# Kernel optimization log

Measured on AMD Instinct MI355X. Metric: run time of the kernel, lower is better.

The kernel has to match this reference:

```python
import jax, jax.numpy as jnp
import numpy as np

# ---- static config (mirrors module init / config constants) ----
STATE_DIM = 512
D_H = 2048
INPUT_DIM = 1024
N_QUBITS = 6
N_VQC_LAYERS = 3
MSD = 128                 # mamba_state_dim (last dim of padded state)
PAD_SLICES = 16           # padded slice count in h_padded
MIN_T = 1e-6              # control_limits.min_value
REL_STEP = 0.1            # control_limits.hardware_relative_step
ABS_STEP = 1e-4           # control_limits.hardware_absolute_step
MAX_T = 0.05              # control_limits.max_value
DIM = 2 ** N_QUBITS

# qubit 0 = most significant bit (matches reshape-based gate application)
_BITS = ((np.arange(DIM)[:, None] >> np.arange(N_QUBITS)[None, ::-1]) & 1).astype(np.float32)
_sign = np.ones(DIM, np.float32)
for k in range(N_QUBITS):  # ring CZ entanglement
    k2 = (k + 1) % N_QUBITS
    _sign *= 1.0 - 2.0 * _BITS[:, k] * _BITS[:, k2]
CZ_SIGN = jnp.asarray(_sign)
Z_OBS = jnp.asarray((1.0 - 2.0 * _BITS).mean(axis=1))  # mean <Z_k> observable weights


def _apply_ry(state, ang, k):
    # state: [B, 2^n] real statevector; ang: [B] rotation angle on qubit k
    B = state.shape[0]
    s = state.reshape(B, 2 ** k, 2, 2 ** (N_QUBITS - k - 1))
    c = jnp.cos(ang / 2)[:, None, None]
    si = jnp.sin(ang / 2)[:, None, None]
    a0, a1 = s[:, :, 0, :], s[:, :, 1, :]
    out = jnp.stack([c * a0 - si * a1, si * a0 + c * a1], axis=2)
    return out.reshape(B, DIM)


def _vqc(feats, enc_W, enc_b, thetas):
    # EvolutionTimeVQCLayer: angle-encode features, layered RY + ring CZ, mean-Z expectation
    B = feats.shape[0]
    angles = feats @ enc_W + enc_b  # [B, n_qubits]
    state = jnp.zeros((B, DIM), feats.dtype).at[:, 0].set(1.0)
    for k in range(N_QUBITS):
        state = _apply_ry(state, angles[:, k], k)
    for l in range(N_VQC_LAYERS):
        for k in range(N_QUBITS):
            state = _apply_ry(state, jnp.broadcast_to(thetas[l, k], (B,)), k)
        state = state * CZ_SIGN[None, :]
    return (state * state) @ Z_OBS  # [B]


def _hamiltonian(q, p, x, W1, b1, W2, b2, W3, b3):
    z = jnp.concatenate([q, p, x], axis=-1)          # [B, 2*S + D]
    h1 = jnp.tanh(z @ W1 + b1)
    h2 = jnp.tanh(h1 @ W2 + b2)
    return (h2 @ W3)[:, 0] + b3                       # [B] scalar energy per sample


def setup_inputs() -> dict:
    key = jax.random.key(0)
    ks = jax.random.split(key, 12)
    def glorot(k, shape):
        std = np.sqrt(2.0 / (shape[0] + shape[-1]))
        return jax.random.normal(k, shape, jnp.float32) * std
    B = 2048
    h_in = 2 * STATE_DIM + INPUT_DIM
    gen_in = INPUT_DIM + 2 * STATE_DIM
    return {
        'x': jax.random.normal(ks[0], (B, INPUT_DIM), jnp.float32),
        'h_padded': jax.random.normal(ks[1], (B, PAD_SLICES, MSD), jnp.float32),
        'aux_padded': jnp.zeros((B, PAD_SLICES, MSD), jnp.float32),
        'W1': glorot(ks[2], (h_in, D_H)), 'b1': jnp.zeros((D_H,), jnp.float32),
        'W2': glorot(ks[3], (D_H, D_H)), 'b2': jnp.zeros((D_H,), jnp.float32),
        'W3': glorot(ks[4], (D_H, 1)), 'b3': jnp.zeros((), jnp.float32),
        'W_out': glorot(ks[5], (2 * STATE_DIM, INPUT_DIM)),
        'b_out': jnp.zeros((INPUT_DIM,), jnp.float32),
        'enc_W': glorot(ks[6], (gen_in, N_QUBITS)) * 0.1,
        'enc_b': jnp.zeros((N_QUBITS,), jnp.float32),
        'thetas': jax.random.normal(ks[7], (N_VQC_LAYERS, N_QUBITS), jnp.float32) * 0.1,
        'gain': jnp.asarray(0.1, jnp.float32),
        'shift': jnp.asarray(7.0, jnp.float32),
        'cap_param': jnp.asarray(0.02, jnp.float32),
        'time_bias': jnp.asarray(0.0005, jnp.float32),
        'last_stable': jnp.asarray(0.0005, jnp.float32),
    }


def reference(x, h_padded, aux_padded, W1, b1, W2, b2, W3, b3, W_out, b_out,
              enc_W, enc_b, thetas, gain, shift, cap_param, time_bias, last_stable):
    B = x.shape[0]
    total = 2 * STATE_DIM
    num_slices = total // MSD
    # unpack phase-space state from padded mamba-shaped state
    unpacked = h_padded[:, :num_slices, :].reshape(B, total)
    q_t, p_t = jnp.split(unpacked, 2, axis=-1)

    # ---- evolution-time generation via VQC ----
    ctrl = jnp.concatenate([x, q_t, p_t], axis=-1)
    samples = _vqc(ctrl, enc_W, enc_b, thetas)                       # [B]
    soft_gain = jax.nn.softplus(gain)
    soft_shift = jax.nn.softplus(shift)
    adjusted = jax.nn.softplus(soft_gain * samples - soft_shift)
    raw = jnp.mean(adjusted) + time_bias
    cap = jnp.maximum(jax.nn.softplus(cap_param), 1e-6)
    evo = cap * jax.nn.sigmoid(raw / cap)
    evo = jnp.where(jnp.isfinite(evo), evo, cap * jax.nn.sigmoid(time_bias / cap))
    prev = jnp.maximum(last_stable, MIN_T)
    cand = jnp.maximum(evo, MIN_T)
    max_step = jnp.maximum(prev * REL_STEP, ABS_STEP)
    cand = jnp.minimum(cand, prev + max_step)
    cand = jnp.minimum(cand, MAX_T)
    dt = jnp.where(jnp.isfinite(cand), cand, prev)                   # scalar

    # ---- fused HNN symplectic (leapfrog) step ----
    def H_sum(q, p):
        return _hamiltonian(q, p, x, W1, b1, W2, b2, W3, b3).sum()
    grad_qp = jax.grad(H_sum, argnums=(0, 1))
    dHdq0, _ = grad_qp(q_t, p_t)
    p_half = p_t - 0.5 * dt * dHdq0
    _, dHdp_h = grad_qp(q_t, p_half)
    q_next = q_t + dt * dHdp_h
    dHdq_n, _ = grad_qp(q_next, p_half)
    p_next = p_half - 0.5 * dt * dHdq_n

    out = jnp.concatenate([q_next, p_next], axis=-1) @ W_out + b_out  # [B, INPUT_DIM]

    # repack state into padded mamba layout
    new_slices = jnp.concatenate([q_next, p_next], axis=-1).reshape(B, num_slices, MSD)
    pad = jnp.zeros((B, PAD_SLICES - num_slices, MSD), out.dtype)
    h_next = jnp.concatenate([new_slices, pad], axis=1)
    return out, h_next
```

## Files before the change

kernel.cpp:

```cpp
#include <hip/hip_runtime.h>
#include <math.h>

#define NB 2048
#define ZD 2048
#define SD 512
#define NELEM_Z (NB * ZD)
#define MB_ (1024 * 1024)

typedef float f32x4 __attribute__((ext_vector_type(4)));
typedef __bf16 bf16x8 __attribute__((ext_vector_type(8)));
typedef __bf16 bf16x4 __attribute__((ext_vector_type(4)));
typedef int i32x4 __attribute__((ext_vector_type(4)));
typedef int i32x8 __attribute__((ext_vector_type(8)));
typedef long long i64;

__device__ __forceinline__ float softplus_f(float x) {
  if (x > 20.f) return x;
  if (x < -20.f) return expf(x);
  return log1pf(expf(x));
}

__device__ __forceinline__ void gload_lds16(const __bf16* g, __bf16* l) {
  __builtin_amdgcn_global_load_lds(
      (__attribute__((address_space(1))) void*)(g),
      (__attribute__((address_space(3))) void*)(l), 16, 0, 0);
}
__device__ __forceinline__ void gload_lds16u(const unsigned char* g,
                                             unsigned char* l) {
  __builtin_amdgcn_global_load_lds(
      (__attribute__((address_space(1))) void*)(g),
      (__attribute__((address_space(3))) void*)(l), 16, 0, 0);
}

__device__ __forceinline__ int pack_fp8x4(float a, float b, float c, float d) {
  int p = __builtin_amdgcn_cvt_pk_fp8_f32(a, b, 0, false);
  p = __builtin_amdgcn_cvt_pk_fp8_f32(c, d, p, true);
  return p;
}
__device__ __forceinline__ float fp8_to_f32(unsigned char b) {
  return __builtin_amdgcn_cvt_f32_fp8((int)b, 0);
}

__global__ __launch_bounds__(256) void build_z_kernel(
    const float* __restrict__ x,
    const float* __restrict__ h_padded,
    const float* __restrict__ enc_W,
    const float* __restrict__ enc_b,
    float* __restrict__ z,
    __bf16* __restrict__ zb,
    unsigned char* __restrict__ zf8,
    float* __restrict__ angles) {
  int b = blockIdx.x;
  int tid = threadIdx.x;
  int lane = tid & 63, w = tid >> 6;
  __shared__ float red[4][6];

  float pa[6] = {0.f, 0.f, 0.f, 0.f, 0.f, 0.f};
#pragma unroll
  for (int cc = 0; cc < 2; cc++) {
    int c = cc * 256 + tid;
    int i = c * 4;
    f32x4 v = (i < 1024) ? ((const f32x4*)(h_padded + (size_t)b * 2048))[c]
                         : ((const f32x4*)(x + (size_t)b * 1024))[c - 256];
    size_t zi = (size_t)b * 512 + c;
    if (cc == 0) {
      ((f32x4*)z)[zi] = v;
      bf16x4 o;
      o[0] = (__bf16)v[0]; o[1] = (__bf16)v[1];
      o[2] = (__bf16)v[2]; o[3] = (__bf16)v[3];
      ((bf16x4*)zb)[zi] = o;
    }
    ((int*)zf8)[zi] = pack_fp8x4(v[0], v[1], v[2], v[3]);
    int cj = (i < 1024) ? (1024 + i) : (i - 1024);
#pragma unroll
    for (int e = 0; e < 4; e++) {
      const float* wp = enc_W + (size_t)(cj + e) * 6;
#pragma unroll
      for (int k = 0; k < 6; k++) pa[k] += v[e] * wp[k];
    }
  }
#pragma unroll
  for (int k = 0; k < 6; k++)
    for (int off = 32; off > 0; off >>= 1) pa[k] += __shfl_down(pa[k], off, 64);
  if (lane == 0) {
#pragma unroll
    for (int k = 0; k < 6; k++) red[w][k] = pa[k];
  }
  __syncthreads();
  if (tid < 6)
    angles[b * 6 + tid] =
        red[0][tid] + red[1][tid] + red[2][tid] + red[3][tid] + enc_b[tid];
}

__global__ void prep_w(const float* __restrict__ in,
                       __bf16* __restrict__ outT, int R, int C) {
  __shared__ float tile[32][33];
  int bx = blockIdx.x * 32, by = blockIdx.y * 32;
  int tx = threadIdx.x, ty = threadIdx.y;
  for (int r = ty; r < 32; r += 8)
    tile[r][tx] = in[(size_t)(by + r) * C + bx + tx];
  __syncthreads();
  for (int r = ty; r < 32; r += 8)
    outT[(size_t)(bx + r) * R + by + tx] = (__bf16)tile[tx][r];
}

__global__ void prep_w8x2(const float* __restrict__ W1,
                          const float* __restrict__ W2,
                          unsigned char* __restrict__ N1,
                          unsigned char* __restrict__ T1,
                          unsigned char* __restrict__ N2,
                          unsigned char* __restrict__ T2) {
  const float* in = blockIdx.z ? W2 : W1;
  unsigned char* outN = blockIdx.z ? N2 : N1;
  unsigned char* outT = blockIdx.z ? T2 : T1;
  const int C = ZD, R = ZD;
  __shared__ float tile[32][33];
  int bx = blockIdx.x * 32, by = blockIdx.y * 32;
  int tx = threadIdx.x, ty = threadIdx.y;
  for (int r = ty; r < 32; r += 8) {
    float v = in[(size_t)(by + r) * C + bx + tx] * 16.f;
    tile[r][tx] = v;
    int p = __builtin_amdgcn_cvt_pk_fp8_f32(v, v, 0, false);
    outN[(size_t)(by + r) * C + bx + tx] = (unsigned char)(p & 0xff);
  }
  __syncthreads();
  for (int r = ty; r < 32; r += 8) {
    float v = tile[tx][r];
    int p = __builtin_amdgcn_cvt_pk_fp8_f32(v, v, 0, false);
    outT[(size_t)(bx + r) * R + by + tx] = (unsigned char)(p & 0xff);
  }
}

__global__ __launch_bounds__(256) void sim_kernel(
    const float* __restrict__ angles,
    const float* __restrict__ thetas,
    const float* __restrict__ gain,
    const float* __restrict__ shift,
    float* __restrict__ partial) {
  const int lane = threadIdx.x & 63;
  const int wv = threadIdx.x >> 6;
  const int row = blockIdx.x * 4 + wv;

  const int rot = ((lane << 1) | (lane >> 5)) & 63;
  const float czs = (__popc(lane & rot) & 1) ? -1.f : 1.f;
  const float zo = (6.f - 2.f * (float)__popc(lane)) * (1.f / 6.f);

  float ang = 0.f;
  if (lane < 6) ang = angles[row * 6 + lane];
  else if (lane < 24) ang = thetas[lane - 6];
  float half = 0.5f * ang;
  float cj = cosf(half), sj = sinf(half);

  float c_arr[24], s_arr[24];
#pragma unroll
  for (int j = 0; j < 24; j++) {
    c_arr[j] = __shfl(cj, j, 64);
    s_arr[j] = __shfl(sj, j, 64);
  }

  float s = (lane == 0) ? 1.f : 0.f;
#pragma unroll
  for (int j = 0; j < 24; j++) {
    const int m = 1 << (5 - (j % 6));
    float t = __shfl_xor(s, m, 64);
    float tt = (lane & m) ? t : -t;
    s = fmaf(c_arr[j], s, s_arr[j] * tt);
    if (j >= 6 && (j % 6) == 5) s *= czs;
  }

  float val = s * s * zo;
#pragma unroll
  for (int off = 32; off > 0; off >>= 1) val += __shfl_xor(val, off, 64);

  __shared__ float red[4];
  if (lane == 0) {
    float sg = softplus_f(gain[0]);
    float ss = softplus_f(shift[0]);
    red[wv] = softplus_f(sg * val - ss);
  }
  __syncthreads();
  if (threadIdx.x == 0)
    partial[blockIdx.x] = red[0] + red[1] + red[2] + red[3];
}

__global__ __launch_bounds__(256) void dt_kernel(
    const float* __restrict__ partial,
    const float* __restrict__ cap_param,
    const float* __restrict__ time_bias,
    const float* __restrict__ last_stable,
    float* __restrict__ dt_out) {
  int tid = threadIdx.x;
  int lane = tid & 63, wv = tid >> 6;
  float v = partial[tid] + partial[tid + 256];
#pragma unroll
  for (int off = 32; off > 0; off >>= 1) v += __shfl_xor(v, off, 64);
  __shared__ float red[4];
  if (lane == 0) red[wv] = v;
  __syncthreads();
  if (tid == 0) {
    float a = red[0] + red[1] + red[2] + red[3];
    float raw = a * (1.f / (float)NB) + time_bias[0];
    float cap = fmaxf(softplus_f(cap_param[0]), 1e-6f);
    float evo = cap / (1.f + expf(-raw / cap));
    if (!isfinite(evo)) evo = cap / (1.f + expf(-time_bias[0] / cap));
    float prev = fmaxf(last_stable[0], 1e-6f);
    float cand = fmaxf(evo, 1e-6f);
    float max_step = fmaxf(prev * 0.1f, 1e-4f);
    cand = fminf(cand, prev + max_step);
    cand = fminf(cand, 0.05f);
    dt_out[0] = isfinite(cand) ? cand : prev;
  }
}

template <int EPI>
__global__ __launch_bounds__(256, 2) void mfma_gemm8(
    const unsigned char* __restrict__ A, int lda,
    const unsigned char* __restrict__ Bt, int ldb,
    void* __restrict__ Cv, int ldc,
    const float* __restrict__ bias,
    const float* __restrict__ w3,
    const unsigned char* __restrict__ aux, int ldaux,
    int Kslice) {
  __shared__ __align__(16) unsigned char sA[2][128 * 128];
  __shared__ __align__(16) unsigned char sB[2][64 * 128];

  const int tid = threadIdx.x;
  const int lane = tid & 63;
  const int w = tid >> 6;
  const int wm = w & 1, wn = w >> 1;
  const int row0 = blockIdx.y * 128;
  const int col0 = blockIdx.x * 64;
  const int koff = blockIdx.z * Kslice;

  const unsigned char* gA[4]; int dA[4];
  const unsigned char* gB[2]; int dB[2];
#pragma unroll
  for (int i = 0; i < 4; i++) {
    int c = i * 256 + tid;
    int m = c >> 3, s = c & 7;
    int l = s ^ (m & 7);
    gA[i] = A + (size_t)(row0 + m) * lda + koff + l * 16;
    dA[i] = c * 16;
  }
#pragma unroll
  for (int i = 0; i < 2; i++) {
    int c = i * 256 + tid;
    int m = c >> 3, s = c & 7;
    int l = s ^ (m & 7);
    gB[i] = Bt + (size_t)(col0 + m) * ldb + koff + l * 16;
    dB[i] = c * 16;
  }

  const int q = lane >> 4, r = lane & 15;
  int aoff[4][2], boff[2][2];
#pragma unroll
  for (int i = 0; i < 4; i++) {
    int ma = wm * 64 + i * 16 + r;
#pragma unroll
    for (int H = 0; H < 2; H++)
      aoff[i][H] = ma * 128 + (((2 * q + H) ^ (ma & 7)) << 4);
  }
#pragma unroll
  for (int j = 0; j < 2; j++) {
    int mb = wn * 32 + j * 16 + r;
#pragma unroll
    for (int H = 0; H < 2; H++)
      boff[j][H] = mb * 128 + (((2 * q + H) ^ (mb & 7)) << 4);
  }

  f32x4 acc[4][2] = {};

#pragma unroll
  for (int i = 0; i < 4; i++) gload_lds16u(gA[i], &sA[0][0] + dA[i]);
#pragma unroll
  for (int i = 0; i < 2; i++) gload_lds16u(gB[i], &sB[0][0] + dB[i]);

  int cur = 0;
  for (int k0 = 0; k0 < Kslice; k0 += 128) {
    __syncthreads();
    if (k0 + 128 < Kslice) {
      int nxt = cur ^ 1;
#pragma unroll
      for (int i = 0; i < 4; i++)
        gload_lds16u(gA[i] + k0 + 128, &sA[nxt][0] + dA[i]);
#pragma unroll
      for (int i = 0; i < 2; i++)
        gload_lds16u(gB[i] + k0 + 128, &sB[nxt][0] + dB[i]);
    }

    const unsigned char* bA = &sA[cur][0];
    const unsigned char* bB = &sB[cur][0];
    i32x8 af[4], bfr[2];
#pragma unroll
    for (int i = 0; i < 4; i++) {
      i32x4 lo = *(const i32x4*)(bA + aoff[i][0]);
      i32x4 hi = *(const i32x4*)(bA + aoff[i][1]);
      af[i] = __builtin_shufflevector(lo, hi, 0, 1, 2, 3, 4, 5, 6, 7);
    }
#pragma unroll
    for (int j = 0; j < 2; j++) {
      i32x4 lo = *(const i32x4*)(bB + boff[j][0]);
      i32x4 hi = *(const i32x4*)(bB + boff[j][1]);
      bfr[j] = __builtin_shufflevector(lo, hi, 0, 1, 2, 3, 4, 5, 6, 7);
    }
#pragma unroll
    for (int i = 0; i < 4; i++)
#pragma unroll
      for (int j = 0; j < 2; j++)
        acc[i][j] = __builtin_amdgcn_mfma_scale_f32_16x16x128_f8f6f4(
            af[i], bfr[j], acc[i][j], 0 , 0 ,
            0, 0x7F7F7F7F, 0, 0x7F7F7F7F);
    cur ^= 1;
  }

  float* Cf = (float*)Cv;
  unsigned char* C8 = (unsigned char*)Cv;
  float* Pz = Cf + (size_t)blockIdx.z * (size_t)gridDim.y * 128 * ldc;

#pragma unroll
  for (int i = 0; i < 4; i++) {
    int rowb = row0 + wm * 64 + i * 16 + q * 4;
#pragma unroll
    for (int j = 0; j < 2; j++) {
      int col = col0 + wn * 32 + j * 16 + r;
      if (EPI == 0) {
#pragma unroll
        for (int g = 0; g < 4; g++)
          Pz[(size_t)(rowb + g) * ldc + col] = acc[i][j][g];
      } else {
        float o[4];
#pragma unroll
        for (int g = 0; g < 4; g++) {
          float v = acc[i][j][g] * 0.0625f;
          if (EPI == 1) {
            o[g] = tanhf(v + bias[col]);
          } else if (EPI == 2) {
            float t = tanhf(v + bias[col]);
            o[g] = 32.f * (1.f - t * t) * w3[col];
          } else {
            float h = fp8_to_f32(aux[(size_t)(rowb + g) * ldaux + col]);
            o[g] = v * (1.f - h * h);
          }
        }
        int p = pack_fp8x4(o[0], o[1], o[2], o[3]);
#pragma unroll
        for (int g = 0; g < 4; g++)
          C8[(size_t)(rowb + g) * ldc + col] =
              (unsigned char)((p >> (8 * g)) & 0xff);
      }
    }
  }
}

__global__ __launch_bounds__(256, 2) void mfma_gemm_bf16(
    const __bf16* __restrict__ A, int lda,
    const __bf16* __restrict__ Bt, int ldb,
    float* __restrict__ P, int ldc,
    int Kslice) {
  __shared__ __bf16 sA[2][128 * 64];
  __shared__ __bf16 sB[2][64 * 64];

  const int tid = threadIdx.x;
  const int lane = tid & 63;
  const int w = tid >> 6;
  const int wm = w & 1, wn = w >> 1;
  const int row0 = blockIdx.y * 128;
  const int col0 = blockIdx.x * 64;
  const int koff = blockIdx.z * Kslice;

  const __bf16* gA[4]; int lofA[4];
  const __bf16* gB[2]; int lofB[2];
#pragma unroll
  for (int i = 0; i < 4; i++) {
    int c = i * 256 + tid;
    int m = c >> 3, cc = c & 7;
    int o = cc ^ (m & 7);
    gA[i] = A + (size_t)(row0 + m) * lda + koff + o * 8;
    lofA[i] = c * 8;
  }
#pragma unroll
  for (int i = 0; i < 2; i++) {
    int c = i * 256 + tid;
    int m = c >> 3, cc = c & 7;
    int o = cc ^ (m & 7);
    gB[i] = Bt + (size_t)(col0 + m) * ldb + koff + o * 8;
    lofB[i] = c * 8;
  }

  const int q = lane >> 4, r = lane & 15;
  int aoff[4][2], boff[2][2];
#pragma unroll
  for (int i = 0; i < 4; i++) {
    int ma = wm * 64 + i * 16 + r;
#pragma unroll
    for (int h = 0; h < 2; h++)
      aoff[i][h] = (ma * 8 + ((h * 4 + q) ^ (ma & 7))) * 8;
  }
#pragma unroll
  for (int j = 0; j < 2; j++) {
    int mb = wn * 32 + j * 16 + r;
#pragma unroll
    for (int h = 0; h < 2; h++)
      boff[j][h] = (mb * 8 + ((h * 4 + q) ^ (mb & 7))) * 8;
  }

  f32x4 acc[4][2] = {};

#pragma unroll
  for (int i = 0; i < 4; i++) gload_lds16(gA[i], &sA[0][0] + lofA[i]);
#pragma unroll
  for (int i = 0; i < 2; i++) gload_lds16(gB[i], &sB[0][0] + lofB[i]);

  int cur = 0;
  for (int k0 = 0; k0 < Kslice; k0 += 64) {
    __syncthreads();
    if (k0 + 64 < Kslice) {
      int nxt = cur ^ 1;
#pragma unroll
      for (int i = 0; i < 4; i++)
        gload_lds16(gA[i] + k0 + 64, &sA[nxt][0] + lofA[i]);
#pragma unroll
      for (int i = 0; i < 2; i++)
        gload_lds16(gB[i] + k0 + 64, &sB[nxt][0] + lofB[i]);
    }
#pragma unroll
    for (int h = 0; h < 2; h++) {
      bf16x8 af[4], bfr[2];
#pragma unroll
      for (int i = 0; i < 4; i++)
        af[i] = *(const bf16x8*)(&sA[cur][0] + aoff[i][h]);
#pragma unroll
      for (int j = 0; j < 2; j++)
        bfr[j] = *(const bf16x8*)(&sB[cur][0] + boff[j][h]);
#pragma unroll
      for (int i = 0; i < 4; i++)
#pragma unroll
        for (int j = 0; j < 2; j++)
          acc[i][j] = __builtin_amdgcn_mfma_f32_16x16x32_bf16(af[i], bfr[j],
                                                              acc[i][j], 0, 0, 0);
    }
    cur ^= 1;
  }

  float* Pz = P + (size_t)blockIdx.z * (size_t)gridDim.y * 128 * ldc;
#pragma unroll
  for (int i = 0; i < 4; i++) {
    int rowb = row0 + wm * 64 + i * 16 + q * 4;
#pragma unroll
    for (int j = 0; j < 2; j++) {
      int col = col0 + wn * 32 + j * 16 + r;
#pragma unroll
      for (int g = 0; g < 4; g++)
        Pz[(size_t)(rowb + g) * ldc + col] = acc[i][j][g];
    }
  }
}

__global__ void update_kernel(float* __restrict__ z, __bf16* __restrict__ zb,
                              unsigned char* __restrict__ zf8,
                              const float* __restrict__ gp,
                              const float* __restrict__ dt,
                              float coef, int off,
                              float* __restrict__ hout) {
  int t = blockIdx.x * blockDim.x + threadIdx.x;
  int b = t >> 7;
  int j4 = t & 127;
  const f32x4* g4 = (const f32x4*)gp;
  constexpr int STRIDE = NB * SD / 4;
  f32x4 g = g4[t] + g4[t + STRIDE] + g4[t + 2 * STRIDE] + g4[t + 3 * STRIDE];
  int zi4 = (b * ZD + off) / 4 + j4;
  f32x4 v = ((f32x4*)z)[zi4];
  float s = coef * dt[0] * (1.f / 512.f);
  v[0] += s * g[0]; v[1] += s * g[1]; v[2] += s * g[2]; v[3] += s * g[3];
  ((f32x4*)z)[zi4] = v;
  bf16x4 o;
  o[0] = (__bf16)v[0]; o[1] = (__bf16)v[1];
  o[2] = (__bf16)v[2]; o[3] = (__bf16)v[3];
  ((bf16x4*)zb)[zi4] = o;
  ((int*)zf8)[zi4] = pack_fp8x4(v[0], v[1], v[2], v[3]);
  if (hout) {
    ((f32x4*)hout)[b * 512 + (off >> 2) + j4] = v;
  }
}

__global__ void wout_reduce(const float* __restrict__ gp,
                            const float* __restrict__ b_out,
                            float* __restrict__ out) {
  int t = blockIdx.x * blockDim.x + threadIdx.x;
  constexpr int S = NB * 1024 / 4;
  const f32x4* g4 = (const f32x4*)gp;
  f32x4 v = g4[t] + g4[t + S];
  f32x4 bb = ((const f32x4*)b_out)[t & 255];
  v[0] += bb[0]; v[1] += bb[1]; v[2] += bb[2]; v[3] += bb[3];
  ((f32x4*)out)[t] = v;
}

__global__ void hzero_kernel(float* __restrict__ out) {
  int t = blockIdx.x * blockDim.x + threadIdx.x;
  int b = t >> 8;
  int j4 = t & 255;
  f32x4 zero = {0.f, 0.f, 0.f, 0.f};
  ((f32x4*)out)[b * 512 + 256 + j4] = zero;
}

extern "C" void kernel_launch(void* const* d_in, const int* in_sizes, int n_in,
                              void* d_out, int out_size, void* d_ws,
                              size_t ws_size, hipStream_t stream) {
  const float* x        = (const float*)d_in[0];
  const float* h_padded = (const float*)d_in[1];
  const float* W1    = (const float*)d_in[3];
  const float* b1    = (const float*)d_in[4];
  const float* W2    = (const float*)d_in[5];
  const float* b2    = (const float*)d_in[6];
  const float* W3    = (const float*)d_in[7];
  const float* W_out = (const float*)d_in[9];
  const float* b_out = (const float*)d_in[10];
  const float* enc_W = (const float*)d_in[11];
  const float* enc_b = (const float*)d_in[12];
  const float* thetas = (const float*)d_in[13];
  const float* gain   = (const float*)d_in[14];
  const float* shift  = (const float*)d_in[15];
  const float* cap_p  = (const float*)d_in[16];
  const float* t_bias = (const float*)d_in[17];
  const float* l_stab = (const float*)d_in[18];

  float* out_mat  = (float*)d_out;
  float* out_hnxt = (float*)d_out + NB * 1024;

  char* base = (char*)d_ws;
  float* z      = (float*)(base);
  float* part   = (float*)(base + 16 * MB_);
  __bf16* zb    = (__bf16*)(base + 32 * MB_);
  __bf16* Wot   = (__bf16*)(base + 40 * MB_);
  float* angl   = (float*)(base + 42 * MB_);
  float* dtp    = (float*)(base + 42 * MB_ + 65536);
  float* simp   = (float*)(base + 42 * MB_ + 80 * 1024);
  unsigned char* zf8  = (unsigned char*)(base + 43 * MB_);
  unsigned char* h1_8 = zf8 + (size_t)NELEM_Z;
  unsigned char* g2_8 = h1_8 + (size_t)NELEM_Z;
  unsigned char* g1_8 = g2_8 + (size_t)NELEM_Z;
  unsigned char* W1n8 = g1_8 + (size_t)NELEM_Z;
  unsigned char* W1t8 = W1n8 + (size_t)NELEM_Z;
  unsigned char* W2n8 = W1t8 + (size_t)NELEM_Z;
  unsigned char* W2t8 = W2n8 + (size_t)NELEM_Z;

  dim3 thr256(256);
  dim3 thrT(32, 8);

  prep_w8x2<<<dim3(64, 64, 2), thrT, 0, stream>>>(W1, W2, W1n8, W1t8, W2n8,
                                                  W2t8);
  prep_w<<<dim3(32, 32), thrT, 0, stream>>>(W_out, Wot, 1024, 1024);

  build_z_kernel<<<dim3(NB), thr256, 0, stream>>>(x, h_padded, enc_W, enc_b, z,
                                                  zb, zf8, angl);
  sim_kernel<<<dim3(NB / 4), thr256, 0, stream>>>(angl, thetas, gain, shift,
                                                  simp);
  dt_kernel<<<dim3(1), thr256, 0, stream>>>(simp, cap_p, t_bias, l_stab, dtp);
  hzero_kernel<<<dim3(NB * 1024 / 4 / 256), thr256, 0, stream>>>(out_hnxt);

  const int   j0r[3]  = {0, 512, 0};
  const int   offs[3] = {512, 0, 512};
  const float coef[3] = {-0.5f, 1.0f, -0.5f};
  float* houts[3];
  houts[0] = nullptr;
  houts[1] = out_hnxt;
  houts[2] = out_hnxt;

  dim3 gridSq(32, 16, 1);
  dim3 gridGr(8, 16, 4);

  for (int i = 0; i < 3; i++) {
    mfma_gemm8<1><<<gridSq, thr256, 0, stream>>>(
        zf8, ZD, W1t8, ZD, h1_8, ZD, b1, nullptr, nullptr, 0, ZD);
    mfma_gemm8<2><<<gridSq, thr256, 0, stream>>>(
        h1_8, ZD, W2t8, ZD, g2_8, ZD, b2, W3, nullptr, 0, ZD);
    mfma_gemm8<3><<<gridSq, thr256, 0, stream>>>(
        g2_8, ZD, W2n8, ZD, g1_8, ZD, nullptr, nullptr, h1_8, ZD, ZD);
    mfma_gemm8<0><<<gridGr, thr256, 0, stream>>>(
        g1_8, ZD, W1n8 + (size_t)j0r[i] * ZD, ZD, part, SD, nullptr, nullptr,
        nullptr, 0, 512);
    update_kernel<<<dim3(NB * SD / 4 / 256), thr256, 0, stream>>>(
        z, zb, zf8, part, dtp, coef[i], offs[i], houts[i]);
  }

  mfma_gemm_bf16<<<dim3(16, 16, 2), thr256, 0, stream>>>(zb, ZD, Wot, 1024,
                                                         part, 1024, 512);
  wout_reduce<<<dim3(NB * 1024 / 4 / 256), thr256, 0, stream>>>(part, b_out,
                                                                out_mat);
}
```

Before: 412.5 us.

## Triple-buffer LDS in FP8 MFMA GEMM with partial vmcnt waits

Moves the FP8 MFMA GEMM main loop from double to triple buffering. Two K-tiles are prefetched ahead, and each iteration waits only for the oldest outstanding loads (vmcnt(6)) instead of draining all of them. The goal is to hide more global-to-LDS latency behind MFMA work. In exchange, LDS per block grows from 48KB to 72KB, which may reduce blocks per CU given launch_bounds(256,2). The loop also assumes Kslice is at least two tiles.

After: 412.7 us. Within noise of the previous version (+0.0%).

```diff
diff --git a/kernel.cpp b/kernel.cpp
--- a/kernel.cpp
+++ b/kernel.cpp
@@ -221,8 +221,8 @@
     const float* __restrict__ w3,
     const unsigned char* __restrict__ aux, int ldaux,
     int Kslice) {
-  __shared__ __align__(16) unsigned char sA[2][128 * 128];
-  __shared__ __align__(16) unsigned char sB[2][64 * 128];
+  __shared__ __align__(16) unsigned char sA[3][128 * 128];
+  __shared__ __align__(16) unsigned char sB[3][64 * 128];
 
   const int tid = threadIdx.x;
   const int lane = tid & 63;
@@ -270,26 +270,17 @@
 
   f32x4 acc[4][2] = {};
 
-#pragma unroll
-  for (int i = 0; i < 4; i++) gload_lds16u(gA[i], &sA[0][0] + dA[i]);
-#pragma unroll
-  for (int i = 0; i < 2; i++) gload_lds16u(gB[i], &sB[0][0] + dB[i]);
-
-  int cur = 0;
-  for (int k0 = 0; k0 < Kslice; k0 += 128) {
-    __syncthreads();
-    if (k0 + 128 < Kslice) {
-      int nxt = cur ^ 1;
-#pragma unroll
-      for (int i = 0; i < 4; i++)
-        gload_lds16u(gA[i] + k0 + 128, &sA[nxt][0] + dA[i]);
-#pragma unroll
-      for (int i = 0; i < 2; i++)
-        gload_lds16u(gB[i] + k0 + 128, &sB[nxt][0] + dB[i]);
-    }
-
-    const unsigned char* bA = &sA[cur][0];
-    const unsigned char* bB = &sB[cur][0];
+  auto issue = [&](int k0, int bi) {
+#pragma unroll
+    for (int i = 0; i < 4; i++)
+      gload_lds16u(gA[i] + k0, &sA[bi][0] + dA[i]);
+#pragma unroll
+    for (int i = 0; i < 2; i++)
+      gload_lds16u(gB[i] + k0, &sB[bi][0] + dB[i]);
+  };
+  auto compute = [&](int bi) {
+    const unsigned char* bA = &sA[bi][0];
+    const unsigned char* bB = &sB[bi][0];
     i32x8 af[4], bfr[2];
 #pragma unroll
     for (int i = 0; i < 4; i++) {
@@ -310,8 +301,24 @@
         acc[i][j] = __builtin_amdgcn_mfma_scale_f32_16x16x128_f8f6f4(
             af[i], bfr[j], acc[i][j], 0 , 0 ,
             0, 0x7F7F7F7F, 0, 0x7F7F7F7F);
-    cur ^= 1;
-  }
+  };
+
+  const int nt = Kslice >> 7;
+
+  issue(0, 0);
+  issue(128, 1);
+
+  for (int t = 0; t < nt - 1; ++t) {
+    asm volatile("s_waitcnt vmcnt(6)" ::: "memory");
+    __builtin_amdgcn_s_barrier();
+    __builtin_amdgcn_sched_barrier(0);
+    if (t + 2 < nt) issue((t + 2) << 7, (t + 2) % 3);
+    compute(t % 3);
+  }
+  asm volatile("s_waitcnt vmcnt(0)" ::: "memory");
+  __builtin_amdgcn_s_barrier();
+  __builtin_amdgcn_sched_barrier(0);
+  compute((nt - 1) % 3);
 
   float* Cf = (float*)Cv;
   unsigned char* C8 = (unsigned char*)Cv;
```
